# Kernel tuning notes

Measured on AMD Instinct MI355X. Metric: run time of the kernel, lower is better.

## Reference

```python
import jax, jax.numpy as jnp
import numpy as np

BETA = 1.0  # cfg.TRAINING.beta
B, S, D = 128, 256, 1024


def setup_inputs() -> dict:
    key = jax.random.key(0)
    k1, k2, k3 = jax.random.split(key, 3)
    bridges = jax.random.normal(k1, (B, S, D), dtype=jnp.float32)
    # monotone increasing timestamps per row (true_divide-safe: bt>bp>bh)
    b_inx = jnp.arange(B * S, dtype=jnp.int32).reshape(B, S)
    # negative indices: one per positive position j in [1, S-2];
    # (idx + 1 + r) % dim guarantees neg_i != i and neg_j != j
    neg_i = (jnp.arange(B, dtype=jnp.int32)[:, None] + 1
             + jax.random.randint(k2, (B, S - 2), 0, B - 1, dtype=jnp.int32)) % B
    neg_j = (jnp.arange(1, S - 1, dtype=jnp.int32)[None, :] + 1
             + jax.random.randint(k3, (B, S - 2), 0, S - 1, dtype=jnp.int32)) % S
    return {"bridges": bridges, "b_inx": b_inx, "neg_i": neg_i, "neg_j": neg_j}


def reference(bridges, b_inx, neg_i, neg_j):
    dt = bridges.dtype
    t = b_inx.astype(dt)
    th = t[:, :1]            # [B,1] head timestamp
    tt = t[:, -1:]           # [B,1] tail timestamp
    tp = t[:, 1:-1]          # [B,S-2] positive timestamps
    alpha = (tp - th) / (tt - th)          # [B,S-2]
    sigma = alpha * (tt - tp)              # [B,S-2]

    head = bridges[:, 0]                   # [B,D]
    tail = bridges[:, -1]                  # [B,D]
    pos = bridges[:, 1:-1]                 # [B,S-2,D]
    neg = bridges[neg_i, neg_j]            # [B,S-2,D]

    a = alpha[..., None]
    mix = (1.0 - a) * head[:, None, :] + a * tail[:, None, :]  # [B,S-2,D]
    xp = pos - mix
    xn = neg - mix
    inv = 1.0 / (2.0 * sigma * sigma)
    pos_dis = -jnp.sum(xp * xp, axis=-1) * inv   # -||x||^2 / (2 sigma^2)
    neg_dis = -jnp.sum(xn * xn, axis=-1) * inv

    cur = pos_dis - neg_dis + jnp.asarray(BETA, dt)
    loss = jnp.sum(jnp.where(cur > 0, cur, jnp.zeros((), dt)))
    return loss / bridges.shape[0]
```

## Files before the change

kernel.cpp:

```cpp
#include <hip/hip_runtime.h>

constexpr int   Bc   = 128;
constexpr int   Sc   = 256;
constexpr int   Dc   = 1024;
constexpr float BETA = 1.0f;

constexpr int WPW   = 8;
constexpr int SLOTS = (Sc - 2 + WPW - 1) / WPW;
constexpr int WAVES = Bc * SLOTS;
constexpr int BLOCK = 256;
constexpr int GRID  = WAVES * 64 / BLOCK;

__global__ __launch_bounds__(BLOCK) void bridge_loss_kernel(
    const float* __restrict__ bridges,
    const int*   __restrict__ b_inx,
    const int*   __restrict__ neg_i,
    const int*   __restrict__ neg_j,
    float*       __restrict__ out)
{
    const int wid  = (blockIdx.x * BLOCK + threadIdx.x) >> 6;
    const int lane = threadIdx.x & 63;
    const int b    = wid / SLOTS;
    const int slot = wid % SLOTS;

    const float th = (float)b_inx[b * Sc];
    const float tt = (float)b_inx[b * Sc + (Sc - 1)];
    const float inv_den = 1.0f / (tt - th);

    const float4* __restrict__ head4 =
        (const float4*)(bridges + (size_t)b * Sc * Dc);
    const float4* __restrict__ tail4 =
        (const float4*)(bridges + ((size_t)b * Sc + (Sc - 1)) * Dc);
    float4 h[4], t[4];
#pragma unroll
    for (int k = 0; k < 4; ++k) {
        h[k] = head4[k * 64 + lane];
        t[k] = tail4[k * 64 + lane];
    }

    float acc = 0.0f;
    const int s0 = 1 + slot * WPW;
    const int s1 = (s0 + WPW < Sc - 1) ? (s0 + WPW) : (Sc - 1);

    for (int s = s0; s < s1; ++s) {
        const float tp    = (float)b_inx[b * Sc + s];
        const float alpha = (tp - th) * inv_den;
        const float sigma = alpha * (tt - tp);
        const float inv   = 1.0f / (2.0f * sigma * sigma);

        const int j  = s - 1;
        const int ni = neg_i[b * (Sc - 2) + j];
        const int nj = neg_j[b * (Sc - 2) + j];

        const float4* __restrict__ pos4 =
            (const float4*)(bridges + ((size_t)b * Sc + s) * Dc);
        const float4* __restrict__ neg4 =
            (const float4*)(bridges + ((size_t)ni * Sc + nj) * Dc);

        float sp = 0.0f, sn = 0.0f;
#pragma unroll
        for (int k = 0; k < 4; ++k) {
            const float4 p = pos4[k * 64 + lane];
            const float4 n = neg4[k * 64 + lane];
            const float m0 = h[k].x + alpha * (t[k].x - h[k].x);
            const float m1 = h[k].y + alpha * (t[k].y - h[k].y);
            const float m2 = h[k].z + alpha * (t[k].z - h[k].z);
            const float m3 = h[k].w + alpha * (t[k].w - h[k].w);
            const float xp0 = p.x - m0, xp1 = p.y - m1, xp2 = p.z - m2, xp3 = p.w - m3;
            const float xn0 = n.x - m0, xn1 = n.y - m1, xn2 = n.z - m2, xn3 = n.w - m3;
            sp += xp0 * xp0 + xp1 * xp1 + xp2 * xp2 + xp3 * xp3;
            sn += xn0 * xn0 + xn1 * xn1 + xn2 * xn2 + xn3 * xn3;
        }

#pragma unroll
        for (int m = 32; m >= 1; m >>= 1) {
            sp += __shfl_xor(sp, m);
            sn += __shfl_xor(sn, m);
        }

        const float cur = (sn - sp) * inv + BETA;
        if (cur > 0.0f) acc += cur;
    }

    if (lane == 0 && acc != 0.0f) {
        atomicAdd(out, acc * (1.0f / (float)Bc));
    }
}

extern "C" void kernel_launch(void* const* d_in, const int* in_sizes, int n_in,
                              void* d_out, int out_size, void* d_ws, size_t ws_size,
                              hipStream_t stream) {
    const float* bridges = (const float*)d_in[0];
    const int*   b_inx   = (const int*)d_in[1];
    const int*   neg_i   = (const int*)d_in[2];
    const int*   neg_j   = (const int*)d_in[3];
    float*       out     = (float*)d_out;

    hipMemsetAsync(out, 0, sizeof(float), stream);

    bridge_loss_kernel<<<GRID, BLOCK, 0, stream>>>(bridges, b_inx, neg_i, neg_j, out);
}
```

Baseline: 242.4 us.

## Double-buffer positive/negative row loads and halve rows per wave

```diff
diff --git a/kernel.cpp b/kernel.cpp
--- a/kernel.cpp
+++ b/kernel.cpp
@@ -5,13 +5,13 @@
 constexpr int   Dc   = 1024;
 constexpr float BETA = 1.0f;
 
-constexpr int WPW   = 8;
+constexpr int WPW   = 4;
 constexpr int SLOTS = (Sc - 2 + WPW - 1) / WPW;
 constexpr int WAVES = Bc * SLOTS;
 constexpr int BLOCK = 256;
-constexpr int GRID  = WAVES * 64 / BLOCK;
+constexpr int GRID  = WAVES / (BLOCK / 64);
 
-__global__ __launch_bounds__(BLOCK) void bridge_loss_kernel(
+__global__ __launch_bounds__(BLOCK, 4) void bridge_loss_kernel(
     const float* __restrict__ bridges,
     const int*   __restrict__ b_inx,
     const int*   __restrict__ neg_i,
@@ -20,67 +20,89 @@
 {
     const int wid  = (blockIdx.x * BLOCK + threadIdx.x) >> 6;
     const int lane = threadIdx.x & 63;
-    const int b    = wid / SLOTS;
-    const int slot = wid % SLOTS;
+    const int b    = wid >> 6;
+    const int slot = wid & (SLOTS - 1);
 
     const float th = (float)b_inx[b * Sc];
     const float tt = (float)b_inx[b * Sc + (Sc - 1)];
     const float inv_den = 1.0f / (tt - th);
 
-    const float4* __restrict__ head4 =
-        (const float4*)(bridges + (size_t)b * Sc * Dc);
-    const float4* __restrict__ tail4 =
-        (const float4*)(bridges + ((size_t)b * Sc + (Sc - 1)) * Dc);
-    float4 h[4], t[4];
+    const int s0    = 1 + slot * WPW;
+    const int rem   = (Sc - 1) - s0;
+    const int nIter = (rem < WPW) ? rem : WPW;
+    const int j0    = s0 - 1;
+
+    float tpv[WPW];
+    int   nrow[WPW];
 #pragma unroll
-    for (int k = 0; k < 4; ++k) {
-        h[k] = head4[k * 64 + lane];
-        t[k] = tail4[k * 64 + lane];
+    for (int i = 0; i < WPW; ++i) {
+        const int ii = (i < nIter) ? i : 0;
+        tpv[i]  = (float)b_inx[b * Sc + s0 + ii];
+        nrow[i] = neg_i[b * (Sc - 2) + j0 + ii] * Sc + neg_j[b * (Sc - 2) + j0 + ii];
+    }
+
+    const float4* __restrict__ row4 = (const float4*)bridges;
+
+    float4 h[4], dt[4];
+    {
+        const float4* hp = row4 + (size_t)(b * Sc) * (Dc / 4);
+        const float4* tp = row4 + (size_t)(b * Sc + Sc - 1) * (Dc / 4);
+#pragma unroll
+        for (int k = 0; k < 4; ++k) {
+            h[k] = hp[k * 64 + lane];
+            float4 t = tp[k * 64 + lane];
+            dt[k] = make_float4(t.x - h[k].x, t.y - h[k].y, t.z - h[k].z, t.w - h[k].w);
+        }
     }
 
     float acc = 0.0f;
-    const int s0 = 1 + slot * WPW;
-    const int s1 = (s0 + WPW < Sc - 1) ? (s0 + WPW) : (Sc - 1);
+    float4 pA[4], nA[4], pB[4], nB[4];
 
-    for (int s = s0; s < s1; ++s) {
-        const float tp    = (float)b_inx[b * Sc + s];
+    auto LOAD = [&](float4 (&P)[4], float4 (&N)[4], int i) {
+        const float4* pp = row4 + (size_t)(b * Sc + s0 + i) * (Dc / 4);
+        const float4* np = row4 + (size_t)nrow[i] * (Dc / 4);
+#pragma unroll
+        for (int k = 0; k < 4; ++k) {
+            P[k] = pp[k * 64 + lane];
+            N[k] = np[k * 64 + lane];
+        }
+    };
+
+    auto COMPUTE = [&](const float4 (&P)[4], const float4 (&N)[4], int i) {
+        const float tp    = tpv[i];
         const float alpha = (tp - th) * inv_den;
         const float sigma = alpha * (tt - tp);
-        const float inv   = 1.0f / (2.0f * sigma * sigma);
-
-        const int j  = s - 1;
-        const int ni = neg_i[b * (Sc - 2) + j];
-        const int nj = neg_j[b * (Sc - 2) + j];
-
-        const float4* __restrict__ pos4 =
-            (const float4*)(bridges + ((size_t)b * Sc + s) * Dc);
-        const float4* __restrict__ neg4 =
-            (const float4*)(bridges + ((size_t)ni * Sc + nj) * Dc);
-
-        float sp = 0.0f, sn = 0.0f;
+        const float invq  = 1.0f / (2.0f * sigma * sigma);
+        float d = 0.0f;
 #pragma unroll
         for (int k = 0; k < 4; ++k) {
-            const float4 p = pos4[k * 64 + lane];
-            const float4 n = neg4[k * 64 + lane];
-            const float m0 = h[k].x + alpha * (t[k].x - h[k].x);
-            const float m1 = h[k].y + alpha * (t[k].y - h[k].y);
-            const float m2 = h[k].z + alpha * (t[k].z - h[k].z);
-            const float m3 = h[k].w + alpha * (t[k].w - h[k].w);
-            const float xp0 = p.x - m0, xp1 = p.y - m1, xp2 = p.z - m2, xp3 = p.w - m3;
-            const float xn0 = n.x - m0, xn1 = n.y - m1, xn2 = n.z - m2, xn3 = n.w - m3;
-            sp += xp0 * xp0 + xp1 * xp1 + xp2 * xp2 + xp3 * xp3;
-            sn += xn0 * xn0 + xn1 * xn1 + xn2 * xn2 + xn3 * xn3;
+            const float m0 = fmaf(alpha, dt[k].x, h[k].x);
+            const float m1 = fmaf(alpha, dt[k].y, h[k].y);
+            const float m2 = fmaf(alpha, dt[k].z, h[k].z);
+            const float m3 = fmaf(alpha, dt[k].w, h[k].w);
+            const float xp0 = P[k].x - m0, xp1 = P[k].y - m1,
+                        xp2 = P[k].z - m2, xp3 = P[k].w - m3;
+            const float xn0 = N[k].x - m0, xn1 = N[k].y - m1,
+                        xn2 = N[k].z - m2, xn3 = N[k].w - m3;
+            d += xn0 * xn0 - xp0 * xp0;
+            d += xn1 * xn1 - xp1 * xp1;
+            d += xn2 * xn2 - xp2 * xp2;
+            d += xn3 * xn3 - xp3 * xp3;
         }
+#pragma unroll
+        for (int msk = 32; msk >= 1; msk >>= 1) d += __shfl_xor(d, msk);
+        const float cur = d * invq + BETA;
+        if (cur > 0.0f) acc += cur;
+    };
 
-#pragma unroll
-        for (int m = 32; m >= 1; m >>= 1) {
-            sp += __shfl_xor(sp, m);
-            sn += __shfl_xor(sn, m);
-        }
-
-        const float cur = (sn - sp) * inv + BETA;
-        if (cur > 0.0f) acc += cur;
-    }
+    LOAD(pA, nA, 0);
+    if (nIter > 1) LOAD(pB, nB, 1);
+    COMPUTE(pA, nA, 0);
+    if (nIter > 2) LOAD(pA, nA, 2);
+    if (nIter > 1) COMPUTE(pB, nB, 1);
+    if (nIter > 3) LOAD(pB, nB, 3);
+    if (nIter > 2) COMPUTE(pA, nA, 2);
+    if (nIter > 3) COMPUTE(pB, nB, 3);
 
     if (lane == 0 && acc != 0.0f) {
         atomicAdd(out, acc * (1.0f / (float)Bc));
```

Result: slower. 268.8 us (+10.9%).

## Invert negative gather into per-row bucket lists so each row is read once

Applied to the files above, without the earlier changes.

```diff
diff --git a/kernel.cpp b/kernel.cpp
--- a/kernel.cpp
+++ b/kernel.cpp
@@ -4,87 +4,164 @@
 constexpr int   Sc   = 256;
 constexpr int   Dc   = 1024;
 constexpr float BETA = 1.0f;
+constexpr int   NP   = Bc * (Sc - 2);
+constexpr int   NR   = Bc * Sc;
 
-constexpr int WPW   = 8;
-constexpr int SLOTS = (Sc - 2 + WPW - 1) / WPW;
-constexpr int WAVES = Bc * SLOTS;
-constexpr int BLOCK = 256;
-constexpr int GRID  = WAVES * 64 / BLOCK;
+constexpr size_t OFF_CNT  = 0;
+constexpr size_t OFF_OFFS = 131072;
+constexpr size_t OFF_SLOT = 262656;
+constexpr size_t OFF_ROW  = 392704;
+constexpr size_t OFF_LIST = 522752;
+constexpr size_t OFF_POS  = 652800;
+constexpr size_t OFF_NEG  = 782848;
 
-__global__ __launch_bounds__(BLOCK) void bridge_loss_kernel(
-    const float* __restrict__ bridges,
-    const int*   __restrict__ b_inx,
-    const int*   __restrict__ neg_i,
-    const int*   __restrict__ neg_j,
-    float*       __restrict__ out)
+__global__ __launch_bounds__(256) void k_build(
+    const int* __restrict__ neg_i, const int* __restrict__ neg_j,
+    int* __restrict__ cnt, int* __restrict__ slotv, int* __restrict__ rowid)
 {
-    const int wid  = (blockIdx.x * BLOCK + threadIdx.x) >> 6;
+    int p = blockIdx.x * 256 + threadIdx.x;
+    if (p >= NP) return;
+    int r = neg_i[p] * Sc + neg_j[p];
+    rowid[p] = r;
+    slotv[p] = atomicAdd(&cnt[r], 1);
+}
+
+__global__ __launch_bounds__(1024) void k_scan(
+    const int* __restrict__ cnt, int* __restrict__ offs)
+{
+    __shared__ int part[1024];
+    const int t = threadIdx.x;
+    const int base = t * 32;
+    int s = 0;
+#pragma unroll
+    for (int i = 0; i < 32; ++i) s += cnt[base + i];
+    part[t] = s;
+    __syncthreads();
+    for (int d = 1; d < 1024; d <<= 1) {
+        int v = (t >= d) ? part[t - d] : 0;
+        __syncthreads();
+        part[t] += v;
+        __syncthreads();
+    }
+    int run = (t == 0) ? 0 : part[t - 1];
+#pragma unroll
+    for (int i = 0; i < 32; ++i) {
+        offs[base + i] = run;
+        run += cnt[base + i];
+    }
+    if (t == 1023) offs[NR] = run;
+}
+
+__global__ __launch_bounds__(256) void k_scatter(
+    const int* __restrict__ offs, const int* __restrict__ slotv,
+    const int* __restrict__ rowid, int* __restrict__ list)
+{
+    int p = blockIdx.x * 256 + threadIdx.x;
+    if (p >= NP) return;
+    int b = p / (Sc - 2);
+    int j = p - b * (Sc - 2);
+    list[offs[rowid[p]] + slotv[p]] = (b << 8) | j;
+}
+
+__global__ __launch_bounds__(256) void k_main(
+    const float* __restrict__ bridges, const int* __restrict__ b_inx,
+    const int* __restrict__ offs, const int* __restrict__ list,
+    float* __restrict__ pos_dis, float* __restrict__ neg_dis)
+{
+    const int wid  = (blockIdx.x * 256 + threadIdx.x) >> 6;
     const int lane = threadIdx.x & 63;
-    const int b    = wid / SLOTS;
-    const int slot = wid % SLOTS;
+    const int r    = wid;
+    const int b    = r >> 8;
+    const int s    = r & 255;
 
-    const float th = (float)b_inx[b * Sc];
-    const float tt = (float)b_inx[b * Sc + (Sc - 1)];
-    const float inv_den = 1.0f / (tt - th);
+    const float4* __restrict__ row4 = (const float4*)bridges;
 
-    const float4* __restrict__ head4 =
-        (const float4*)(bridges + (size_t)b * Sc * Dc);
-    const float4* __restrict__ tail4 =
-        (const float4*)(bridges + ((size_t)b * Sc + (Sc - 1)) * Dc);
-    float4 h[4], t[4];
+    float4 x[4];
+    {
+        const float4* rp = row4 + (size_t)r * (Dc / 4);
 #pragma unroll
-    for (int k = 0; k < 4; ++k) {
-        h[k] = head4[k * 64 + lane];
-        t[k] = tail4[k * 64 + lane];
+        for (int k = 0; k < 4; ++k) x[k] = rp[k * 64 + lane];
     }
 
-    float acc = 0.0f;
-    const int s0 = 1 + slot * WPW;
-    const int s1 = (s0 + WPW < Sc - 1) ? (s0 + WPW) : (Sc - 1);
+    const int beg = offs[r], end = offs[r + 1];
 
-    for (int s = s0; s < s1; ++s) {
-        const float tp    = (float)b_inx[b * Sc + s];
-        const float alpha = (tp - th) * inv_den;
+    if (s >= 1 && s <= Sc - 2) {
+        const float th = (float)b_inx[b * Sc];
+        const float tt = (float)b_inx[b * Sc + (Sc - 1)];
+        const float tp = (float)b_inx[b * Sc + s];
+        const float alpha = (tp - th) / (tt - th);
         const float sigma = alpha * (tt - tp);
         const float inv   = 1.0f / (2.0f * sigma * sigma);
-
-        const int j  = s - 1;
-        const int ni = neg_i[b * (Sc - 2) + j];
-        const int nj = neg_j[b * (Sc - 2) + j];
-
-        const float4* __restrict__ pos4 =
-            (const float4*)(bridges + ((size_t)b * Sc + s) * Dc);
-        const float4* __restrict__ neg4 =
-            (const float4*)(bridges + ((size_t)ni * Sc + nj) * Dc);
-
-        float sp = 0.0f, sn = 0.0f;
+        const float4* hp = row4 + (size_t)(b * Sc) * (Dc / 4);
+        const float4* tq = row4 + (size_t)(b * Sc + Sc - 1) * (Dc / 4);
+        float d = 0.0f;
 #pragma unroll
         for (int k = 0; k < 4; ++k) {
-            const float4 p = pos4[k * 64 + lane];
-            const float4 n = neg4[k * 64 + lane];
-            const float m0 = h[k].x + alpha * (t[k].x - h[k].x);
-            const float m1 = h[k].y + alpha * (t[k].y - h[k].y);
-            const float m2 = h[k].z + alpha * (t[k].z - h[k].z);
-            const float m3 = h[k].w + alpha * (t[k].w - h[k].w);
-            const float xp0 = p.x - m0, xp1 = p.y - m1, xp2 = p.z - m2, xp3 = p.w - m3;
-            const float xn0 = n.x - m0, xn1 = n.y - m1, xn2 = n.z - m2, xn3 = n.w - m3;
-            sp += xp0 * xp0 + xp1 * xp1 + xp2 * xp2 + xp3 * xp3;
-            sn += xn0 * xn0 + xn1 * xn1 + xn2 * xn2 + xn3 * xn3;
+            const float4 h = hp[k * 64 + lane];
+            const float4 t = tq[k * 64 + lane];
+            const float m0 = fmaf(alpha, t.x - h.x, h.x);
+            const float m1 = fmaf(alpha, t.y - h.y, h.y);
+            const float m2 = fmaf(alpha, t.z - h.z, h.z);
+            const float m3 = fmaf(alpha, t.w - h.w, h.w);
+            const float e0 = x[k].x - m0, e1 = x[k].y - m1;
+            const float e2 = x[k].z - m2, e3 = x[k].w - m3;
+            d += e0 * e0 + e1 * e1 + e2 * e2 + e3 * e3;
         }
-
 #pragma unroll
-        for (int m = 32; m >= 1; m >>= 1) {
-            sp += __shfl_xor(sp, m);
-            sn += __shfl_xor(sn, m);
-        }
-
-        const float cur = (sn - sp) * inv + BETA;
-        if (cur > 0.0f) acc += cur;
+        for (int m = 32; m >= 1; m >>= 1) d += __shfl_xor(d, m);
+        if (lane == 0) pos_dis[b * (Sc - 2) + (s - 1)] = -d * inv;
     }
 
-    if (lane == 0 && acc != 0.0f) {
-        atomicAdd(out, acc * (1.0f / (float)Bc));
+    for (int q = beg; q < end; ++q) {
+        const int e  = list[q];
+        const int bb = e >> 8;
+        const int jj = e & 255;
+        const int ss = jj + 1;
+        const float th = (float)b_inx[bb * Sc];
+        const float tt = (float)b_inx[bb * Sc + (Sc - 1)];
+        const float tp = (float)b_inx[bb * Sc + ss];
+        const float alpha = (tp - th) / (tt - th);
+        const float sigma = alpha * (tt - tp);
+        const float inv   = 1.0f / (2.0f * sigma * sigma);
+        const float4* hp = row4 + (size_t)(bb * Sc) * (Dc / 4);
+        const float4* tq = row4 + (size_t)(bb * Sc + Sc - 1) * (Dc / 4);
+        float d = 0.0f;
+#pragma unroll
+        for (int k = 0; k < 4; ++k) {
+            const float4 h = hp[k * 64 + lane];
+            const float4 t = tq[k * 64 + lane];
+            const float m0 = fmaf(alpha, t.x - h.x, h.x);
+            const float m1 = fmaf(alpha, t.y - h.y, h.y);
+            const float m2 = fmaf(alpha, t.z - h.z, h.z);
+            const float m3 = fmaf(alpha, t.w - h.w, h.w);
+            const float e0 = x[k].x - m0, e1 = x[k].y - m1;
+            const float e2 = x[k].z - m2, e3 = x[k].w - m3;
+            d += e0 * e0 + e1 * e1 + e2 * e2 + e3 * e3;
+        }
+#pragma unroll
+        for (int m = 32; m >= 1; m >>= 1) d += __shfl_xor(d, m);
+        if (lane == 0) neg_dis[bb * (Sc - 2) + jj] = -d * inv;
     }
+}
+
+__global__ __launch_bounds__(1024) void k_reduce(
+    const float* __restrict__ pos_dis, const float* __restrict__ neg_dis,
+    float* __restrict__ out)
+{
+    __shared__ float red[1024];
+    const int t = threadIdx.x;
+    float a = 0.0f;
+    for (int p = t; p < NP; p += 1024) {
+        const float cur = pos_dis[p] - neg_dis[p] + BETA;
+        if (cur > 0.0f) a += cur;
+    }
+    red[t] = a;
+    __syncthreads();
+    for (int d = 512; d > 0; d >>= 1) {
+        if (t < d) red[t] += red[t + d];
+        __syncthreads();
+    }
+    if (t == 0) out[0] = red[0] * (1.0f / (float)Bc);
 }
 
 extern "C" void kernel_launch(void* const* d_in, const int* in_sizes, int n_in,
@@ -96,7 +173,19 @@
     const int*   neg_j   = (const int*)d_in[3];
     float*       out     = (float*)d_out;
 
-    hipMemsetAsync(out, 0, sizeof(float), stream);
+    char* ws = (char*)d_ws;
+    int*   cnt     = (int*)(ws + OFF_CNT);
+    int*   offs    = (int*)(ws + OFF_OFFS);
+    int*   slotv   = (int*)(ws + OFF_SLOT);
+    int*   rowid   = (int*)(ws + OFF_ROW);
+    int*   list    = (int*)(ws + OFF_LIST);
+    float* pos_dis = (float*)(ws + OFF_POS);
+    float* neg_dis = (float*)(ws + OFF_NEG);
 
-    bridge_loss_kernel<<<GRID, BLOCK, 0, stream>>>(bridges, b_inx, neg_i, neg_j, out);
+    hipMemsetAsync(cnt, 0, NR * sizeof(int), stream);
+    k_build  <<<(NP + 255) / 256, 256, 0, stream>>>(neg_i, neg_j, cnt, slotv, rowid);
+    k_scan   <<<1, 1024, 0, stream>>>(cnt, offs);
+    k_scatter<<<(NP + 255) / 256, 256, 0, stream>>>(offs, slotv, rowid, list);
+    k_main   <<<NR / 4, 256, 0, stream>>>(bridges, b_inx, offs, list, pos_dis, neg_dis);
+    k_reduce <<<1, 1024, 0, stream>>>(pos_dis, neg_dis, out);
 }
```

Measured after the change: 227.6 us. -6.1%, faster.
